# Performance work log

Measured on AMD Instinct MI355X. Metric: run time of the kernel, lower is better.

Reference implementation:

```python
import jax, jax.numpy as jnp
import numpy as np

Q, P = 32, 32          # output / input channels per node
N1, N2 = 64, 64        # per-dimension quadrature grid sizes (d = 2)
B = 16                 # batch
HID = 128              # MLP hidden width (kernel_layers = [128, 128])


def _mlp_K(y, x, Ws, bs):
    """Per-dimension NN kernel: K[a, c, i, j] = MLP([y_i, x_j])[a*P + c].

    Returns the Khatri-Rao component of shape (Q, P, n_out, n_in).
    """
    n_out, n_in = y.shape[0], x.shape[0]
    feats = jnp.stack([jnp.broadcast_to(y[:, None], (n_out, n_in)),
                       jnp.broadcast_to(x[None, :], (n_out, n_in))], axis=-1)  # (n_out, n_in, 2)
    h = feats
    for W, b in zip(Ws[:-1], bs[:-1]):
        h = jax.nn.gelu(h @ W + b)
    out = h @ Ws[-1] + bs[-1]  # (n_out, n_in, Q*P)
    return out.reshape(n_out, n_in, Q, P).transpose(2, 3, 0, 1)


def setup_inputs() -> dict:
    key = jax.random.key(0)
    ks = jax.random.split(key, 12)

    def w(k, shape):
        return jax.random.normal(k, shape, jnp.float32) / np.float32(np.sqrt(shape[0]))

    return {
        "u":  jax.random.normal(ks[0], (B, P * N1 * N2), jnp.float32),
        "x1": jax.random.uniform(ks[1], (N1,), jnp.float32),   # quadrature points dim 1
        "x2": jax.random.uniform(ks[2], (N2,), jnp.float32),   # quadrature points dim 2
        "w1": jax.random.uniform(ks[3], (N1,), jnp.float32) / N1,  # quadrature weights dim 1
        "w2": jax.random.uniform(ks[4], (N2,), jnp.float32) / N2,  # quadrature weights dim 2
        "k1_W0": w(ks[5], (2, HID)),    "k1_b0": jnp.zeros((HID,), jnp.float32),
        "k1_W1": w(ks[6], (HID, HID)),  "k1_b1": jnp.zeros((HID,), jnp.float32),
        "k1_W2": w(ks[7], (HID, Q * P)), "k1_b2": jnp.zeros((Q * P,), jnp.float32),
        "k2_W0": w(ks[8], (2, HID)),    "k2_b0": jnp.zeros((HID,), jnp.float32),
        "k2_W1": w(ks[9], (HID, HID)),  "k2_b1": jnp.zeros((HID,), jnp.float32),
        "k2_W2": w(ks[10], (HID, Q * P)), "k2_b2": jnp.zeros((Q * P,), jnp.float32),
    }


def reference(u, x1, x2, w1, w2,
              k1_W0, k1_b0, k1_W1, k1_b1, k1_W2, k1_b2,
              k2_W0, k2_b0, k2_W1, k2_b1, k2_W2, k2_b2):
    # Khatri-Rao components, one per spatial dimension
    K1 = _mlp_K(x1, x1, [k1_W0, k1_W1, k1_W2], [k1_b0, k1_b1, k1_b2])  # (Q, P, N1, N1)
    K2 = _mlp_K(x2, x2, [k2_W0, k2_W1, k2_W2], [k2_b0, k2_b1, k2_b2])  # (Q, P, N2, N2)

    # (I_p kron diag(w1 kron w2)) @ u^T  ==  per-channel quadrature weighting
    v = u.reshape(B, P, N1, N2)
    vw = v * w1[None, None, :, None] * w2[None, None, None, :]

    # Block (a, c) of the full kernel is K1[a, c] kron K2[a, c]; apply it as two
    # mode-products without ever materializing the (Q*N, P*N) dense matrix.
    Z1 = jnp.einsum('acij,bcjm->bacim', K1, vw)    # contract dim-1 input index j
    out = jnp.einsum('ackm,bacim->baik', K2, Z1)   # contract dim-2 index m, sum channels c
    return out.reshape(B, Q * N1 * N2)
```

## Files before the change

### kernel.cpp

```cpp
#include <hip/hip_runtime.h>
#include <cmath>

namespace {

typedef short short8 __attribute__((ext_vector_type(8)));
typedef float f32x4  __attribute__((ext_vector_type(4)));
typedef unsigned short ushort;

constexpr int HID  = 128;
constexpr int QP   = 1024;
constexpr int N    = 64;
constexpr int NPTS = 4096;
constexpr int B    = 16;
constexpr int P    = 32;
constexpr int Q    = 32;
constexpr int LDH  = 136;
constexpr int CH   = 4;
constexpr int CCH  = P / CH;

__device__ __forceinline__ ushort f2bf(float x) {
    unsigned u = __float_as_uint(x);
    u += 0x7FFF + ((u >> 16) & 1);
    return (ushort)(u >> 16);
}
__device__ __forceinline__ float bf2f(ushort b) {
    return __uint_as_float((unsigned)b << 16);
}
__device__ __forceinline__ float gelu_tanh(float x) {
    const float c0 = 0.7978845608028654f;
    const float c1 = 0.044715f;
    float inner = c0 * (x + c1 * x * x * x);
    return 0.5f * x * (1.0f + tanhf(inner));
}
__device__ __forceinline__ void gll16(const ushort* src, ushort* dst) {
    __builtin_amdgcn_global_load_lds(
        (const __attribute__((address_space(1))) unsigned int*)src,
        (__attribute__((address_space(3))) unsigned int*)dst, 16, 0, 0);
}

__global__ __launch_bounds__(256)
void prep_kernel(const float* __restrict__ W1a, const float* __restrict__ W2a,
                 const float* __restrict__ W1b, const float* __restrict__ W2b,
                 const float* __restrict__ u,
                 ushort* __restrict__ W1Th, ushort* __restrict__ W1Tl,
                 ushort* __restrict__ W2Th, ushort* __restrict__ W2Tl,
                 ushort* __restrict__ ubf)
{
    const int bid = blockIdx.x;
    if (bid < 1152) {
        const int g   = bid * 256 + threadIdx.x;
        const int dim = g / 147456;
        const int r   = g - dim * 147456;
        const float* W1 = dim ? W1b : W1a;
        const float* W2 = dim ? W2b : W2a;
        float v; ushort *dh, *dl; int idx;
        if (r < 16384) {
            const int o = r >> 7, k = r & 127;
            v = W1[k * HID + o];
            idx = dim * 16384 + r;
            dh = W1Th; dl = W1Tl;
        } else {
            const int r2 = r - 16384;
            const int o = r2 >> 7, k = r2 & 127;
            v = W2[k * QP + o];
            idx = dim * 131072 + r2;
            dh = W2Th; dl = W2Tl;
        }
        const ushort h = f2bf(v);
        const ushort l = f2bf(v - bf2f(h));
        dh[idx] = h; dl[idx] = l;
    } else {
        const int g = (bid - 1152) * 256 + threadIdx.x;
        const float4 v = reinterpret_cast<const float4*>(u)[g];
        uint2 pk;
        pk.x = (unsigned)f2bf(v.x) | ((unsigned)f2bf(v.y) << 16);
        pk.y = (unsigned)f2bf(v.z) | ((unsigned)f2bf(v.w) << 16);
        reinterpret_cast<uint2*>(ubf)[g] = pk;
    }
}

__global__ __launch_bounds__(256, 2)
void mlp_h_kernel(const float* __restrict__ xs1, const float* __restrict__ xs2,
                  const float* __restrict__ W0a, const float* __restrict__ b0a,
                  const float* __restrict__ b1a,
                  const float* __restrict__ W0b, const float* __restrict__ b0b,
                  const float* __restrict__ b1b,
                  const ushort* __restrict__ W1Th, const ushort* __restrict__ W1Tl,
                  ushort* __restrict__ h1h_g, ushort* __restrict__ h1l_g)
{
    __shared__ ushort h0h[N * LDH], h0l[N * LDH];

    const int i   = blockIdx.x;
    const int dim = blockIdx.y;
    const float* xs = dim ? xs2 : xs1;
    const float* W0 = dim ? W0b : W0a;
    const float* b0 = dim ? b0b : b0a;
    const float* b1 = dim ? b1b : b1a;
    const ushort* w1h = W1Th + dim * 16384;
    const ushort* w1l = W1Tl + dim * 16384;

    const int t  = threadIdx.x;
    const int w  = t >> 6;
    const int l  = t & 63;
    const int lr = l & 15;
    const int lh = l >> 4;
    const float y = xs[i];

    {
        const int ch    = t & 127;
        const int pbase = (t >> 7) * 32;
        const float wy = W0[ch], wx = W0[HID + ch], bb = b0[ch];
        for (int pp = 0; pp < 32; ++pp) {
            const int pt = pbase + pp;
            const float z = fmaf(y, wy, fmaf(xs[pt], wx, bb));
            const float h = gelu_tanh(z);
            const ushort hb = f2bf(h);
            h0h[pt * LDH + ch] = hb;
            h0l[pt * LDH + ch] = f2bf(h - bf2f(hb));
        }
    }
    __syncthreads();

    ushort* dh = h1h_g + (size_t)((dim * 64 + i) * 64) * HID;
    ushort* dl = h1l_g + (size_t)((dim * 64 + i) * 64) * HID;
    #pragma unroll
    for (int cc = 0; cc < 2; ++cc) {
        const int ct = w * 2 + cc;
        const ushort* ap = w1h + (ct * 16 + lr) * HID + lh * 8;
        const ushort* aq = w1l + (ct * 16 + lr) * HID + lh * 8;
        short8 Ah[4], Al[4];
        #pragma unroll
        for (int kk = 0; kk < 4; ++kk) {
            Ah[kk] = *reinterpret_cast<const short8*>(ap + kk * 32);
            Al[kk] = *reinterpret_cast<const short8*>(aq + kk * 32);
        }
        f32x4 acc[4];
        #pragma unroll
        for (int p = 0; p < 4; ++p) acc[p] = f32x4{0.f, 0.f, 0.f, 0.f};
        #pragma unroll
        for (int kk = 0; kk < 4; ++kk) {
            short8 Bh[4], Bl[4];
            #pragma unroll
            for (int p = 0; p < 4; ++p) {
                Bh[p] = *reinterpret_cast<const short8*>(&h0h[(p * 16 + lr) * LDH + kk * 32 + lh * 8]);
                Bl[p] = *reinterpret_cast<const short8*>(&h0l[(p * 16 + lr) * LDH + kk * 32 + lh * 8]);
            }
            #pragma unroll
            for (int p = 0; p < 4; ++p)
                acc[p] = __builtin_amdgcn_mfma_f32_16x16x32_bf16(Ah[kk], Bh[p], acc[p], 0, 0, 0);
            #pragma unroll
            for (int p = 0; p < 4; ++p)
                acc[p] = __builtin_amdgcn_mfma_f32_16x16x32_bf16(Al[kk], Bh[p], acc[p], 0, 0, 0);
            #pragma unroll
            for (int p = 0; p < 4; ++p)
                acc[p] = __builtin_amdgcn_mfma_f32_16x16x32_bf16(Ah[kk], Bl[p], acc[p], 0, 0, 0);
        }
        const float4 bb = *reinterpret_cast<const float4*>(&b1[ct * 16 + lh * 4]);
        #pragma unroll
        for (int p = 0; p < 4; ++p) {
            ushort hb[4], lb[4];
            #pragma unroll
            for (int r = 0; r < 4; ++r) {
                const float zv = acc[p][r] + ((const float*)&bb)[r];
                const float h  = gelu_tanh(zv);
                hb[r] = f2bf(h);
                lb[r] = f2bf(h - bf2f(hb[r]));
            }
            uint2 ph, pl;
            ph.x = (unsigned)hb[0] | ((unsigned)hb[1] << 16);
            ph.y = (unsigned)hb[2] | ((unsigned)hb[3] << 16);
            pl.x = (unsigned)lb[0] | ((unsigned)lb[1] << 16);
            pl.y = (unsigned)lb[2] | ((unsigned)lb[3] << 16);
            const size_t off = (size_t)(p * 16 + lr) * HID + ct * 16 + lh * 4;
            *reinterpret_cast<uint2*>(dh + off) = ph;
            *reinterpret_cast<uint2*>(dl + off) = pl;
        }
    }
}

__global__ __launch_bounds__(256, 2)
void mlp_l2_kernel(const ushort* __restrict__ h1h_g, const ushort* __restrict__ h1l_g,
                   const ushort* __restrict__ W2Th, const ushort* __restrict__ W2Tl,
                   const float* __restrict__ b2a, const float* __restrict__ b2b,
                   const float* __restrict__ qw1, const float* __restrict__ qw2,
                   ushort* __restrict__ K1out, ushort* __restrict__ K2out)
{
    const int i   = blockIdx.x;
    const int dim = blockIdx.y;
    const int oz  = blockIdx.z;
    const float* b2 = dim ? b2b : b2a;
    const float* wq = dim ? qw2 : qw1;
    const ushort* w2h = W2Th + dim * 131072;
    const ushort* w2l = W2Tl + dim * 131072;
    ushort* Kout = dim ? K2out : K1out;

    const int t  = threadIdx.x;
    const int w  = t >> 6;
    const int l  = t & 63;
    const int lr = l & 15;
    const int lh = l >> 4;

    const ushort* hh = h1h_g + (size_t)((dim * 64 + i) * 64) * HID;
    const ushort* hl = h1l_g + (size_t)((dim * 64 + i) * 64) * HID;
    short8 Ah[4][4], Al[4][4];
    #pragma unroll
    for (int p = 0; p < 4; ++p)
        #pragma unroll
        for (int kk = 0; kk < 4; ++kk) {
            const size_t off = (size_t)(p * 16 + lr) * HID + kk * 32 + lh * 8;
            Ah[p][kk] = *reinterpret_cast<const short8*>(hh + off);
            Al[p][kk] = *reinterpret_cast<const short8*>(hl + off);
        }

    const int otbase = oz * 16 + w * 4;

#define LOADB(BH, BL, OT) do {                                                      \
        const ushort* _p = w2h + (size_t)((OT) * 16 + lr) * HID + lh * 8;           \
        const ushort* _q = w2l + (size_t)((OT) * 16 + lr) * HID + lh * 8;           \
        _Pragma("unroll")                                                           \
        for (int kk = 0; kk < 4; ++kk) {                                            \
            BH[kk] = *reinterpret_cast<const short8*>(_p + kk * 32);                \
            BL[kk] = *reinterpret_cast<const short8*>(_q + kk * 32);                \
        } } while (0)

#define MMTILE(BH, BL, OT) do {                                                     \
        f32x4 acc[4];                                                               \
        _Pragma("unroll")                                                           \
        for (int p = 0; p < 4; ++p) acc[p] = f32x4{0.f, 0.f, 0.f, 0.f};             \
        _Pragma("unroll")                                                           \
        for (int kk = 0; kk < 4; ++kk) {                                            \
            _Pragma("unroll")                                                       \
            for (int p = 0; p < 4; ++p)                                             \
                acc[p] = __builtin_amdgcn_mfma_f32_16x16x32_bf16(Ah[p][kk], BH[kk], acc[p], 0, 0, 0); \
            _Pragma("unroll")                                                       \
            for (int p = 0; p < 4; ++p)                                             \
                acc[p] = __builtin_amdgcn_mfma_f32_16x16x32_bf16(Al[p][kk], BH[kk], acc[p], 0, 0, 0); \
            _Pragma("unroll")                                                       \
            for (int p = 0; p < 4; ++p)                                             \
                acc[p] = __builtin_amdgcn_mfma_f32_16x16x32_bf16(Ah[p][kk], BL[kk], acc[p], 0, 0, 0); \
        }                                                                           \
        const int _o = (OT) * 16 + lr;                                              \
        const float _bo = b2[_o];                                                   \
        ushort* _d = Kout + (size_t)_o * NPTS + i * 64 + lh * 4;                    \
        _Pragma("unroll")                                                           \
        for (int p = 0; p < 4; ++p) {                                               \
            const float4 _wv = *reinterpret_cast<const float4*>(wq + p * 16 + lh * 4); \
            uint2 pk;                                                               \
            pk.x = (unsigned)f2bf((acc[p][0] + _bo) * _wv.x) |                      \
                   ((unsigned)f2bf((acc[p][1] + _bo) * _wv.y) << 16);               \
            pk.y = (unsigned)f2bf((acc[p][2] + _bo) * _wv.z) |                      \
                   ((unsigned)f2bf((acc[p][3] + _bo) * _wv.w) << 16);               \
            *reinterpret_cast<uint2*>(_d + p * 16) = pk;                            \
        } } while (0)

    short8 B0h[4], B0l[4], B1h[4], B1l[4];
    LOADB(B0h, B0l, otbase + 0);
    LOADB(B1h, B1l, otbase + 1);
    MMTILE(B0h, B0l, otbase + 0);
    LOADB(B0h, B0l, otbase + 2);
    MMTILE(B1h, B1l, otbase + 1);
    LOADB(B1h, B1l, otbase + 3);
    MMTILE(B0h, B0l, otbase + 2);
    MMTILE(B1h, B1l, otbase + 3);
#undef LOADB
#undef MMTILE
}

__global__ __launch_bounds__(256, 2)
void contract_kernel(const ushort* __restrict__ ubf,
                     const ushort* __restrict__ K1,
                     const ushort* __restrict__ K2,
                     float* __restrict__ part)
{
    __shared__ ushort sK1[2][4096];
    __shared__ ushort sK2[2][4096];
    __shared__ ushort sZT[4][4096];

    const int id0 = blockIdx.x;
    const int id  = (id0 & 7) * 64 + (id0 >> 3);
    const int bg  = id & 3;
    const int a   = (id >> 2) & 31;
    const int ch  = id >> 7;

    const int t  = threadIdx.x;
    const int w  = t >> 6;
    const int l  = t & 63;
    const int lr = l & 15;
    const int lh = l >> 4;
    const int b  = bg * 4 + w;
    const int c0 = ch * CCH;

    ushort* zt = &sZT[w][0];
    const int sc = (((l & 7) ^ (l >> 3)) << 3);
    const int r0 = 16 * w + (l >> 3);

#define STAGE(NB, CC) do {                                                      \
        const ushort* _k1 = K1 + (((size_t)a * P + (CC)) << 12);                \
        const ushort* _k2 = K2 + (((size_t)a * P + (CC)) << 12);                \
        gll16(_k1 + (r0    ) * 64 + sc, &sK1[NB][w * 1024      ]);              \
        gll16(_k1 + (r0 + 8) * 64 + sc, &sK1[NB][w * 1024 + 512]);              \
        gll16(_k2 + (r0    ) * 64 + sc, &sK2[NB][w * 1024      ]);              \
        gll16(_k2 + (r0 + 8) * 64 + sc, &sK2[NB][w * 1024 + 512]);              \
    } while (0)

#define LOAD_UF(CC) do {                                                        \
        const ushort* _up = ubf + (((size_t)b * P + (CC)) << 12);               \
        _Pragma("unroll")                                                       \
        for (int jt = 0; jt < 4; ++jt)                                          \
            _Pragma("unroll")                                                   \
            for (int kk = 0; kk < 2; ++kk)                                      \
                UF[jt][kk] = *reinterpret_cast<const short8*>(                  \
                    _up + (16 * jt + lr) * 64 + kk * 32 + lh * 8);              \
    } while (0)

#define MM1(BUF) do {                                                           \
        short8 Bf[4][2];                                                        \
        _Pragma("unroll")                                                       \
        for (int kt = 0; kt < 4; ++kt)                                          \
            _Pragma("unroll")                                                   \
            for (int kk = 0; kk < 2; ++kk)                                      \
                Bf[kt][kk] = *reinterpret_cast<const short8*>(                  \
                    &sK2[BUF][(16 * kt + lr) * 64 + (((kk * 4 + lh) ^ (lr & 7)) << 3)]); \
        _Pragma("unroll")                                                       \
        for (int jt = 0; jt < 4; ++jt)                                          \
            _Pragma("unroll")                                                   \
            for (int kt = 0; kt < 4; ++kt) zacc[jt][kt] = f32x4{0.f, 0.f, 0.f, 0.f}; \
        _Pragma("unroll")                                                       \
        for (int kk = 0; kk < 2; ++kk)                                          \
            _Pragma("unroll")                                                   \
            for (int jt = 0; jt < 4; ++jt)                                      \
                _Pragma("unroll")                                               \
                for (int kt = 0; kt < 4; ++kt)                                  \
                    zacc[jt][kt] = __builtin_amdgcn_mfma_f32_16x16x32_bf16(     \
                        UF[jt][kk], Bf[kt][kk], zacc[jt][kt], 0, 0, 0);         \
    } while (0)

#define ZTW() do {                                                              \
        _Pragma("unroll")                                                       \
        for (int kt = 0; kt < 4; ++kt) {                                        \
            const int rbase = (16 * kt + lr) * 64;                              \
            _Pragma("unroll")                                                   \
            for (int jt = 0; jt < 4; ++jt) {                                    \
                const f32x4 z = zacc[jt][kt];                                   \
                uint2 pk;                                                       \
                pk.x = (unsigned)f2bf(z[0]) | ((unsigned)f2bf(z[1]) << 16);     \
                pk.y = (unsigned)f2bf(z[2]) | ((unsigned)f2bf(z[3]) << 16);     \
                const int g = (2 * jt + (lh >> 1)) ^ (lr & 7);                  \
                *reinterpret_cast<uint2*>(&zt[rbase + (g << 3) + (lh & 1) * 4]) = pk; \
            }                                                                   \
        }                                                                       \
    } while (0)

#define MM2(BUF) do {                                                           \
        _Pragma("unroll")                                                       \
        for (int jj = 0; jj < 2; ++jj) {                                        \
            short8 A2[4], B2[4];                                                \
            _Pragma("unroll")                                                   \
            for (int it = 0; it < 4; ++it)                                      \
                A2[it] = *reinterpret_cast<const short8*>(                      \
                    &sK1[BUF][(16 * it + lr) * 64 + (((jj * 4 + lh) ^ (lr & 7)) << 3)]); \
            _Pragma("unroll")                                                   \
            for (int kt = 0; kt < 4; ++kt)                                      \
                B2[kt] = *reinterpret_cast<const short8*>(                      \
                    &zt[(16 * kt + lr) * 64 + (((jj * 4 + lh) ^ (lr & 7)) << 3)]); \
            _Pragma("unroll")                                                   \
            for (int it = 0; it < 4; ++it)                                      \
                _Pragma("unroll")                                               \
                for (int kt = 0; kt < 4; ++kt)                                  \
                    oacc[it][kt] = __builtin_amdgcn_mfma_f32_16x16x32_bf16(     \
                        A2[it], B2[kt], oacc[it][kt], 0, 0, 0);                 \
        }                                                                       \
    } while (0)

    f32x4 oacc[4][4];
    #pragma unroll
    for (int it = 0; it < 4; ++it)
        #pragma unroll
        for (int kt = 0; kt < 4; ++kt) oacc[it][kt] = f32x4{0.f, 0.f, 0.f, 0.f};
    f32x4 zacc[4][4];
    short8 UF[4][2];

    STAGE(0, c0);
    STAGE(1, c0 + 1);
    LOAD_UF(c0);
    __syncthreads();
    MM1(0);

    #pragma unroll
    for (int cc = 0; cc < CCH; ++cc) {
        ZTW();
        if (cc + 1 < CCH) LOAD_UF(c0 + cc + 1);
        asm volatile("s_waitcnt lgkmcnt(0)" ::: "memory");
        __builtin_amdgcn_sched_barrier(0);
        MM2(cc & 1);
        if (cc + 1 < CCH) {
            __syncthreads();
            MM1((cc + 1) & 1);
            if (cc + 2 < CCH) STAGE(cc & 1, c0 + cc + 2);
        }
    }

#undef STAGE
#undef LOAD_UF
#undef MM1
#undef ZTW
#undef MM2

    float* pp = part + ((((size_t)ch * B + b) * Q + a) << 12);
    #pragma unroll
    for (int it = 0; it < 4; ++it)
        #pragma unroll
        for (int kt = 0; kt < 4; ++kt)
            #pragma unroll
            for (int r = 0; r < 4; ++r)
                pp[(16 * it + 4 * lh + r) * 64 + 16 * kt + lr] = oacc[it][kt][r];
}

__global__ __launch_bounds__(256)
void addparts_kernel(const float* __restrict__ part, float* __restrict__ out)
{
    const int g = blockIdx.x * 256 + threadIdx.x;
    constexpr size_t SLAB = (size_t)B * Q * NPTS / 4;
    const float4* p = reinterpret_cast<const float4*>(part);
    float4 s0 = p[g];
    float4 s1 = p[g + SLAB];
    float4 s2 = p[g + 2 * SLAB];
    float4 s3 = p[g + 3 * SLAB];
    float4 r;
    r.x = (s0.x + s1.x) + (s2.x + s3.x);
    r.y = (s0.y + s1.y) + (s2.y + s3.y);
    r.z = (s0.z + s1.z) + (s2.z + s3.z);
    r.w = (s0.w + s1.w) + (s2.w + s3.w);
    reinterpret_cast<float4*>(out)[g] = r;
}

}

extern "C" void kernel_launch(void* const* d_in, const int* in_sizes, int n_in,
                              void* d_out, int out_size, void* d_ws, size_t ws_size,
                              hipStream_t stream)
{
    const float* u     = (const float*)d_in[0];
    const float* x1    = (const float*)d_in[1];
    const float* x2    = (const float*)d_in[2];
    const float* w1    = (const float*)d_in[3];
    const float* w2    = (const float*)d_in[4];
    const float* k1W0  = (const float*)d_in[5];
    const float* k1b0  = (const float*)d_in[6];
    const float* k1W1  = (const float*)d_in[7];
    const float* k1b1  = (const float*)d_in[8];
    const float* k1W2  = (const float*)d_in[9];
    const float* k1b2  = (const float*)d_in[10];
    const float* k2W0  = (const float*)d_in[11];
    const float* k2b0  = (const float*)d_in[12];
    const float* k2W1  = (const float*)d_in[13];
    const float* k2b1  = (const float*)d_in[14];
    const float* k2W2  = (const float*)d_in[15];
    const float* k2b2  = (const float*)d_in[16];

    float* out = (float*)d_out;
    char* ws = (char*)d_ws;
    size_t off = 0;
    ushort* K1buf = (ushort*)(ws + off); off += (size_t)QP * NPTS * 2;
    ushort* K2buf = (ushort*)(ws + off); off += (size_t)QP * NPTS * 2;
    ushort* W2Th  = (ushort*)(ws + off); off += 2 * 131072 * 2;
    ushort* W2Tl  = (ushort*)(ws + off); off += 2 * 131072 * 2;
    ushort* W1Th  = (ushort*)(ws + off); off += 2 * 16384 * 2;
    ushort* W1Tl  = (ushort*)(ws + off); off += 2 * 16384 * 2;
    ushort* ubf   = (ushort*)(ws + off); off += (size_t)B * P * NPTS * 2;
    float*  part  = (float*)(ws + off);  off += (size_t)CH * B * Q * NPTS * 4;
    ushort* h1h_g = (ushort*)(ws + off); off += (size_t)2 * 64 * 64 * HID * 2;
    ushort* h1l_g = (ushort*)(ws + off); off += (size_t)2 * 64 * 64 * HID * 2;

    prep_kernel<<<dim3(3200), 256, 0, stream>>>(
        k1W1, k1W2, k2W1, k2W2, u, W1Th, W1Tl, W2Th, W2Tl, ubf);

    mlp_h_kernel<<<dim3(64, 2), 256, 0, stream>>>(
        x1, x2,
        k1W0, k1b0, k1b1,
        k2W0, k2b0, k2b1,
        W1Th, W1Tl,
        h1h_g, h1l_g);

    mlp_l2_kernel<<<dim3(64, 2, 4), 256, 0, stream>>>(
        h1h_g, h1l_g, W2Th, W2Tl, k1b2, k2b2, w1, w2, K1buf, K2buf);

    contract_kernel<<<dim3(512), 256, 0, stream>>>(ubf, K1buf, K2buf, part);

    addparts_kernel<<<dim3((B * Q * NPTS) / (256 * 4)), 256, 0, stream>>>(part, out);
}
```

Before: 76.87 us.

## Fuse MLP hidden and output layers into one kernel; restructure contract pipeline

Merges the two MLP kernels into one, so the second hidden layer stays in shared memory instead of being written to and re-read from global memory, and one launch is removed. Each block now covers 32 output tiles instead of 16 over a 64x2x2 grid, and the first two layers are recomputed twice per (i,dim). The contract kernel's stage/MM1/MM2 loop is reordered with double-buffered U fragments and s_setprio around the MFMA bursts, aiming for better overlap of loads and compute. Trade-offs: lower occupancy (launch bounds 256,1), more shared memory, and fewer blocks in the MLP stage.

```diff
diff --git a/kernel.cpp b/kernel.cpp
--- a/kernel.cpp
+++ b/kernel.cpp
@@ -79,25 +79,34 @@
     }
 }
 
-__global__ __launch_bounds__(256, 2)
-void mlp_h_kernel(const float* __restrict__ xs1, const float* __restrict__ xs2,
-                  const float* __restrict__ W0a, const float* __restrict__ b0a,
-                  const float* __restrict__ b1a,
-                  const float* __restrict__ W0b, const float* __restrict__ b0b,
-                  const float* __restrict__ b1b,
-                  const ushort* __restrict__ W1Th, const ushort* __restrict__ W1Tl,
-                  ushort* __restrict__ h1h_g, ushort* __restrict__ h1l_g)
+__global__ __launch_bounds__(256, 1)
+void mlp_kernel(const float* __restrict__ xs1, const float* __restrict__ xs2,
+                const float* __restrict__ W0a, const float* __restrict__ b0a,
+                const float* __restrict__ b1a, const float* __restrict__ b2a,
+                const float* __restrict__ W0b, const float* __restrict__ b0b,
+                const float* __restrict__ b1b, const float* __restrict__ b2b,
+                const ushort* __restrict__ W1Th, const ushort* __restrict__ W1Tl,
+                const ushort* __restrict__ W2Th, const ushort* __restrict__ W2Tl,
+                const float* __restrict__ qw1, const float* __restrict__ qw2,
+                ushort* __restrict__ K1out, ushort* __restrict__ K2out)
 {
     __shared__ ushort h0h[N * LDH], h0l[N * LDH];
+    __shared__ ushort h1h[N * LDH], h1l[N * LDH];
 
     const int i   = blockIdx.x;
     const int dim = blockIdx.y;
+    const int bz  = blockIdx.z;
     const float* xs = dim ? xs2 : xs1;
     const float* W0 = dim ? W0b : W0a;
     const float* b0 = dim ? b0b : b0a;
     const float* b1 = dim ? b1b : b1a;
+    const float* b2 = dim ? b2b : b2a;
+    const float* wq = dim ? qw2 : qw1;
     const ushort* w1h = W1Th + dim * 16384;
     const ushort* w1l = W1Tl + dim * 16384;
+    const ushort* w2h = W2Th + dim * 131072;
+    const ushort* w2l = W2Tl + dim * 131072;
+    ushort* Kout = dim ? K2out : K1out;
 
     const int t  = threadIdx.x;
     const int w  = t >> 6;
@@ -121,98 +130,74 @@
     }
     __syncthreads();
 
-    ushort* dh = h1h_g + (size_t)((dim * 64 + i) * 64) * HID;
-    ushort* dl = h1l_g + (size_t)((dim * 64 + i) * 64) * HID;
-    #pragma unroll
-    for (int cc = 0; cc < 2; ++cc) {
-        const int ct = w * 2 + cc;
-        const ushort* ap = w1h + (ct * 16 + lr) * HID + lh * 8;
-        const ushort* aq = w1l + (ct * 16 + lr) * HID + lh * 8;
-        short8 Ah[4], Al[4];
+    {
         #pragma unroll
-        for (int kk = 0; kk < 4; ++kk) {
-            Ah[kk] = *reinterpret_cast<const short8*>(ap + kk * 32);
-            Al[kk] = *reinterpret_cast<const short8*>(aq + kk * 32);
-        }
-        f32x4 acc[4];
-        #pragma unroll
-        for (int p = 0; p < 4; ++p) acc[p] = f32x4{0.f, 0.f, 0.f, 0.f};
-        #pragma unroll
-        for (int kk = 0; kk < 4; ++kk) {
-            short8 Bh[4], Bl[4];
+        for (int cc = 0; cc < 2; ++cc) {
+            const int ct = w * 2 + cc;
+            const ushort* ap = w1h + (ct * 16 + lr) * HID + lh * 8;
+            const ushort* aq = w1l + (ct * 16 + lr) * HID + lh * 8;
+            short8 Ah[4], Al[4];
+            #pragma unroll
+            for (int kk = 0; kk < 4; ++kk) {
+                Ah[kk] = *reinterpret_cast<const short8*>(ap + kk * 32);
+                Al[kk] = *reinterpret_cast<const short8*>(aq + kk * 32);
+            }
+            f32x4 acc[4];
+            #pragma unroll
+            for (int p = 0; p < 4; ++p) acc[p] = f32x4{0.f, 0.f, 0.f, 0.f};
+            #pragma unroll
+            for (int kk = 0; kk < 4; ++kk) {
+                short8 Bh[4], Bl[4];
+                #pragma unroll
+                for (int p = 0; p < 4; ++p) {
+                    Bh[p] = *reinterpret_cast<const short8*>(&h0h[(p * 16 + lr) * LDH + kk * 32 + lh * 8]);
+                    Bl[p] = *reinterpret_cast<const short8*>(&h0l[(p * 16 + lr) * LDH + kk * 32 + lh * 8]);
+                }
+                #pragma unroll
+                for (int p = 0; p < 4; ++p)
+                    acc[p] = __builtin_amdgcn_mfma_f32_16x16x32_bf16(Ah[kk], Bh[p], acc[p], 0, 0, 0);
+                #pragma unroll
+                for (int p = 0; p < 4; ++p)
+                    acc[p] = __builtin_amdgcn_mfma_f32_16x16x32_bf16(Al[kk], Bh[p], acc[p], 0, 0, 0);
+                #pragma unroll
+                for (int p = 0; p < 4; ++p)
+                    acc[p] = __builtin_amdgcn_mfma_f32_16x16x32_bf16(Ah[kk], Bl[p], acc[p], 0, 0, 0);
+            }
+            const float4 bb = *reinterpret_cast<const float4*>(&b1[ct * 16 + lh * 4]);
             #pragma unroll
             for (int p = 0; p < 4; ++p) {
-                Bh[p] = *reinterpret_cast<const short8*>(&h0h[(p * 16 + lr) * LDH + kk * 32 + lh * 8]);
-                Bl[p] = *reinterpret_cast<const short8*>(&h0l[(p * 16 + lr) * LDH + kk * 32 + lh * 8]);
+                ushort hb[4], lb[4];
+                #pragma unroll
+                for (int r = 0; r < 4; ++r) {
+                    const float zv = acc[p][r] + ((const float*)&bb)[r];
+                    const float h  = gelu_tanh(zv);
+                    hb[r] = f2bf(h);
+                    lb[r] = f2bf(h - bf2f(hb[r]));
+                }
+                uint2 ph, pl;
+                ph.x = (unsigned)hb[0] | ((unsigned)hb[1] << 16);
+                ph.y = (unsigned)hb[2] | ((unsigned)hb[3] << 16);
+                pl.x = (unsigned)lb[0] | ((unsigned)lb[1] << 16);
+                pl.y = (unsigned)lb[2] | ((unsigned)lb[3] << 16);
+                const int off = (p * 16 + lr) * LDH + ct * 16 + lh * 4;
+                *reinterpret_cast<uint2*>(&h1h[off]) = ph;
+                *reinterpret_cast<uint2*>(&h1l[off]) = pl;
             }
-            #pragma unroll
-            for (int p = 0; p < 4; ++p)
-                acc[p] = __builtin_amdgcn_mfma_f32_16x16x32_bf16(Ah[kk], Bh[p], acc[p], 0, 0, 0);
-            #pragma unroll
-            for (int p = 0; p < 4; ++p)
-                acc[p] = __builtin_amdgcn_mfma_f32_16x16x32_bf16(Al[kk], Bh[p], acc[p], 0, 0, 0);
-            #pragma unroll
-            for (int p = 0; p < 4; ++p)
-                acc[p] = __builtin_amdgcn_mfma_f32_16x16x32_bf16(Ah[kk], Bl[p], acc[p], 0, 0, 0);
-        }
-        const float4 bb = *reinterpret_cast<const float4*>(&b1[ct * 16 + lh * 4]);
-        #pragma unroll
-        for (int p = 0; p < 4; ++p) {
-            ushort hb[4], lb[4];
-            #pragma unroll
-            for (int r = 0; r < 4; ++r) {
-                const float zv = acc[p][r] + ((const float*)&bb)[r];
-                const float h  = gelu_tanh(zv);
-                hb[r] = f2bf(h);
-                lb[r] = f2bf(h - bf2f(hb[r]));
-            }
-            uint2 ph, pl;
-            ph.x = (unsigned)hb[0] | ((unsigned)hb[1] << 16);
-            ph.y = (unsigned)hb[2] | ((unsigned)hb[3] << 16);
-            pl.x = (unsigned)lb[0] | ((unsigned)lb[1] << 16);
-            pl.y = (unsigned)lb[2] | ((unsigned)lb[3] << 16);
-            const size_t off = (size_t)(p * 16 + lr) * HID + ct * 16 + lh * 4;
-            *reinterpret_cast<uint2*>(dh + off) = ph;
-            *reinterpret_cast<uint2*>(dl + off) = pl;
         }
     }
-}
-
-__global__ __launch_bounds__(256, 2)
-void mlp_l2_kernel(const ushort* __restrict__ h1h_g, const ushort* __restrict__ h1l_g,
-                   const ushort* __restrict__ W2Th, const ushort* __restrict__ W2Tl,
-                   const float* __restrict__ b2a, const float* __restrict__ b2b,
-                   const float* __restrict__ qw1, const float* __restrict__ qw2,
-                   ushort* __restrict__ K1out, ushort* __restrict__ K2out)
-{
-    const int i   = blockIdx.x;
-    const int dim = blockIdx.y;
-    const int oz  = blockIdx.z;
-    const float* b2 = dim ? b2b : b2a;
-    const float* wq = dim ? qw2 : qw1;
-    const ushort* w2h = W2Th + dim * 131072;
-    const ushort* w2l = W2Tl + dim * 131072;
-    ushort* Kout = dim ? K2out : K1out;
-
-    const int t  = threadIdx.x;
-    const int w  = t >> 6;
-    const int l  = t & 63;
-    const int lr = l & 15;
-    const int lh = l >> 4;
-
-    const ushort* hh = h1h_g + (size_t)((dim * 64 + i) * 64) * HID;
-    const ushort* hl = h1l_g + (size_t)((dim * 64 + i) * 64) * HID;
-    short8 Ah[4][4], Al[4][4];
-    #pragma unroll
-    for (int p = 0; p < 4; ++p)
+    __syncthreads();
+
+    {
+        short8 Ah[4][4], Al[4][4];
         #pragma unroll
-        for (int kk = 0; kk < 4; ++kk) {
-            const size_t off = (size_t)(p * 16 + lr) * HID + kk * 32 + lh * 8;
-            Ah[p][kk] = *reinterpret_cast<const short8*>(hh + off);
-            Al[p][kk] = *reinterpret_cast<const short8*>(hl + off);
-        }
-
-    const int otbase = oz * 16 + w * 4;
+        for (int p = 0; p < 4; ++p)
+            #pragma unroll
+            for (int kk = 0; kk < 4; ++kk) {
+                Ah[p][kk] = *reinterpret_cast<const short8*>(&h1h[(p * 16 + lr) * LDH + kk * 32 + lh * 8]);
+                Al[p][kk] = *reinterpret_cast<const short8*>(&h1l[(p * 16 + lr) * LDH + kk * 32 + lh * 8]);
+            }
+
+        const int otbase = bz * 32 + w * 8;
 
 #define LOADB(BH, BL, OT) do {                                                      \
         const ushort* _p = w2h + (size_t)((OT) * 16 + lr) * HID + lh * 8;           \
@@ -253,17 +238,18 @@
             *reinterpret_cast<uint2*>(_d + p * 16) = pk;                            \
         } } while (0)
 
-    short8 B0h[4], B0l[4], B1h[4], B1l[4];
-    LOADB(B0h, B0l, otbase + 0);
-    LOADB(B1h, B1l, otbase + 1);
-    MMTILE(B0h, B0l, otbase + 0);
-    LOADB(B0h, B0l, otbase + 2);
-    MMTILE(B1h, B1l, otbase + 1);
-    LOADB(B1h, B1l, otbase + 3);
-    MMTILE(B0h, B0l, otbase + 2);
-    MMTILE(B1h, B1l, otbase + 3);
+        short8 B0h[4], B0l[4], B1h[4], B1l[4];
+        LOADB(B0h, B0l, otbase + 0);
+        #pragma unroll
+        for (int oo = 0; oo < 8; oo += 2) {
+            if (oo + 1 < 8) LOADB(B1h, B1l, otbase + oo + 1);
+            MMTILE(B0h, B0l, otbase + oo);
+            if (oo + 2 < 8) LOADB(B0h, B0l, otbase + oo + 2);
+            MMTILE(B1h, B1l, otbase + oo + 1);
+        }
 #undef LOADB
 #undef MMTILE
+    }
 }
 
 __global__ __launch_bounds__(256, 2)
@@ -303,7 +289,7 @@
         gll16(_k2 + (r0 + 8) * 64 + sc, &sK2[NB][w * 1024 + 512]);              \
     } while (0)
 
-#define LOAD_UF(CC) do {                                                        \
+#define LOAD_UF(UF, CC) do {                                                    \
         const ushort* _up = ubf + (((size_t)b * P + (CC)) << 12);               \
         _Pragma("unroll")                                                       \
         for (int jt = 0; jt < 4; ++jt)                                          \
@@ -313,7 +299,7 @@
                     _up + (16 * jt + lr) * 64 + kk * 32 + lh * 8);              \
     } while (0)
 
-#define MM1(BUF) do {                                                           \
+#define MM1(BUF, UF) do {                                                       \
         short8 Bf[4][2];                                                        \
         _Pragma("unroll")                                                       \
         for (int kt = 0; kt < 4; ++kt)                                          \
@@ -325,6 +311,7 @@
         for (int jt = 0; jt < 4; ++jt)                                          \
             _Pragma("unroll")                                                   \
             for (int kt = 0; kt < 4; ++kt) zacc[jt][kt] = f32x4{0.f, 0.f, 0.f, 0.f}; \
+        __builtin_amdgcn_s_setprio(1);                                          \
         _Pragma("unroll")                                                       \
         for (int kk = 0; kk < 2; ++kk)                                          \
             _Pragma("unroll")                                                   \
@@ -333,6 +320,7 @@
                 for (int kt = 0; kt < 4; ++kt)                                  \
                     zacc[jt][kt] = __builtin_amdgcn_mfma_f32_16x16x32_bf16(     \
                         UF[jt][kk], Bf[kt][kk], zacc[jt][kt], 0, 0, 0);         \
+        __builtin_amdgcn_s_setprio(0);                                          \
     } while (0)
 
 #define ZTW() do {                                                              \
@@ -363,12 +351,14 @@
             for (int kt = 0; kt < 4; ++kt)                                      \
                 B2[kt] = *reinterpret_cast<const short8*>(                      \
                     &zt[(16 * kt + lr) * 64 + (((jj * 4 + lh) ^ (lr & 7)) << 3)]); \
+            __builtin_amdgcn_s_setprio(1);                                      \
             _Pragma("unroll")                                                   \
             for (int it = 0; it < 4; ++it)                                      \
                 _Pragma("unroll")                                               \
                 for (int kt = 0; kt < 4; ++kt)                                  \
                     oacc[it][kt] = __builtin_amdgcn_mfma_f32_16x16x32_bf16(     \
                         A2[it], B2[kt], oacc[it][kt], 0, 0, 0);                 \
+            __builtin_amdgcn_s_setprio(0);                                      \
         }                                                                       \
     } while (0)
 
@@ -378,26 +368,28 @@
         #pragma unroll
         for (int kt = 0; kt < 4; ++kt) oacc[it][kt] = f32x4{0.f, 0.f, 0.f, 0.f};
     f32x4 zacc[4][4];
-    short8 UF[4][2];
+    short8 UFa[4][2], UFb[4][2];
 
     STAGE(0, c0);
-    STAGE(1, c0 + 1);
-    LOAD_UF(c0);
+    LOAD_UF(UFa, c0);
     __syncthreads();
-    MM1(0);
 
     #pragma unroll
     for (int cc = 0; cc < CCH; ++cc) {
+        const int cur = cc & 1;
+        if (cc + 1 < CCH) STAGE(cur ^ 1, c0 + cc + 1);
+        if (cur == 0) {
+            MM1(0, UFa);
+            if (cc + 1 < CCH) LOAD_UF(UFb, c0 + cc + 1);
+        } else {
+            MM1(1, UFb);
+            if (cc + 1 < CCH) LOAD_UF(UFa, c0 + cc + 1);
+        }
         ZTW();
-        if (cc + 1 < CCH) LOAD_UF(c0 + cc + 1);
         asm volatile("s_waitcnt lgkmcnt(0)" ::: "memory");
         __builtin_amdgcn_sched_barrier(0);
-        MM2(cc & 1);
-        if (cc + 1 < CCH) {
-            __syncthreads();
-            MM1((cc + 1) & 1);
-            if (cc + 2 < CCH) STAGE(cc & 1, c0 + cc + 2);
-        }
+        MM2(cur);
+        __syncthreads();
     }
 
 #undef STAGE
@@ -469,21 +461,17 @@
     ushort* W1Tl  = (ushort*)(ws + off); off += 2 * 16384 * 2;
     ushort* ubf   = (ushort*)(ws + off); off += (size_t)B * P * NPTS * 2;
     float*  part  = (float*)(ws + off);  off += (size_t)CH * B * Q * NPTS * 4;
-    ushort* h1h_g = (ushort*)(ws + off); off += (size_t)2 * 64 * 64 * HID * 2;
-    ushort* h1l_g = (ushort*)(ws + off); off += (size_t)2 * 64 * 64 * HID * 2;
 
     prep_kernel<<<dim3(3200), 256, 0, stream>>>(
         k1W1, k1W2, k2W1, k2W2, u, W1Th, W1Tl, W2Th, W2Tl, ubf);
 
-    mlp_h_kernel<<<dim3(64, 2), 256, 0, stream>>>(
+    mlp_kernel<<<dim3(64, 2, 2), 256, 0, stream>>>(
         x1, x2,
-        k1W0, k1b0, k1b1,
-        k2W0, k2b0, k2b1,
-        W1Th, W1Tl,
-        h1h_g, h1l_g);
-
-    mlp_l2_kernel<<<dim3(64, 2, 4), 256, 0, stream>>>(
-        h1h_g, h1l_g, W2Th, W2Tl, k1b2, k2b2, w1, w2, K1buf, K2buf);
+        k1W0, k1b0, k1b1, k1b2,
+        k2W0, k2b0, k2b1, k2b2,
+        W1Th, W1Tl, W2Th, W2Tl,
+        w1, w2,
+        K1buf, K2buf);
 
     contract_kernel<<<dim3(512), 256, 0, stream>>>(ubf, K1buf, K2buf, part);
 
```

Measured after the change: 67.12 us. -12.7%, faster.
